# Optimization experiments

Hardware: AMD Instinct MI355X
Metric: run time of the kernel (lower is better)

Reference implementation:

```python
import jax, jax.numpy as jnp
import numpy as np

B, C, N = 4, 128, 25000
E = 200000            # edges per graph
H, DH = 4, 32         # heads, per-head dim
OUT = H * DH          # 128
ED = 32               # edge feature dim


def setup_inputs() -> dict:
    key = jax.random.key(0)
    ks = jax.random.split(key, 16)
    s = 0.05
    return {
        'x': jax.random.normal(ks[0], (B, C, N, 1), jnp.float32),
        'edge_index': jax.random.randint(ks[1], (B, 2, E), 0, B * N, jnp.int64),
        'edge_attr': jax.random.normal(ks[2], (B * E, ED), jnp.float32),
        'Wq': jax.random.normal(ks[3], (C, OUT), jnp.float32) * s,
        'bq': jnp.zeros((OUT,), jnp.float32),
        'Wk': jax.random.normal(ks[4], (C, OUT), jnp.float32) * s,
        'bk': jnp.zeros((OUT,), jnp.float32),
        'Wv': jax.random.normal(ks[5], (C, OUT), jnp.float32) * s,
        'bv': jnp.zeros((OUT,), jnp.float32),
        'We': jax.random.normal(ks[6], (ED, OUT), jnp.float32) * s,
        'Wskip': jax.random.normal(ks[7], (C, OUT), jnp.float32) * s,
        'bskip': jnp.zeros((OUT,), jnp.float32),
        'W1': jax.random.normal(ks[8], (OUT, 2 * OUT), jnp.float32) * s,
        'b1': jnp.zeros((2 * OUT,), jnp.float32),
        'W2': jax.random.normal(ks[9], (2 * OUT, OUT), jnp.float32) * s,
        'b2': jnp.zeros((OUT,), jnp.float32),
    }


def reference(x, edge_index, edge_attr, Wq, bq, Wk, bk, Wv, bv, We,
              Wskip, bskip, W1, b1, W2, b2):
    b, c, n, _ = x.shape
    nb = b * n
    # [B,C,N,1] -> [B*N, C]
    xf = x.squeeze(-1).transpose(0, 2, 1).reshape(nb, c)
    # [B,2,E] -> [2, B*E]
    ei = edge_index.transpose(1, 0, 2).reshape(2, -1)
    src, dst = ei[0], ei[1]

    q = (xf @ Wq + bq).reshape(nb, H, DH)
    k = (xf @ Wk + bk).reshape(nb, H, DH)
    v = (xf @ Wv + bv).reshape(nb, H, DH)
    e = (edge_attr @ We).reshape(-1, H, DH)  # [T,H,DH]

    qi = q[dst]            # gather target queries  [T,H,DH]
    kj = k[src] + e        # gather source keys + edge proj
    vj = v[src] + e

    scale = 1.0 / np.sqrt(DH).astype(np.float32)
    alpha = (qi * kj).sum(-1) * scale  # [T,H]

    # segment softmax over edges sharing a destination node
    amax = jax.ops.segment_max(alpha, dst, num_segments=nb)
    amax = jnp.where(jnp.isfinite(amax), amax, 0.0)
    ea = jnp.exp(alpha - amax[dst])
    denom = jax.ops.segment_sum(ea, dst, num_segments=nb)
    attn = ea / (denom[dst] + 1e-16)   # [T,H]

    agg = jax.ops.segment_sum(vj * attn[..., None], dst, num_segments=nb)
    out = agg.reshape(nb, OUT) + (xf @ Wskip + bskip)  # root skip

    # feed-forward + final activation
    h = jnp.maximum(out @ W1 + b1, 0.0) @ W2 + b2
    h = jnp.maximum(h, 0.0)

    # [B*N, OUT] -> [B, OUT, N, 1]
    return h.reshape(b, n, OUT).transpose(0, 2, 1)[..., None]
```

## Files before the change

### kernel.cpp

```cpp
#include <hip/hip_runtime.h>
#include <hip/hip_bf16.h>

#define NB      100000
#define NPB     25000
#define T_E     800000
#define EPG     200000
#define DMODEL  128
#define EDIM    32
#define FFD     256
#define SCAN_NBLK 98

typedef __attribute__((ext_vector_type(8))) short bf16x8;
typedef __attribute__((ext_vector_type(4))) float f32x4;
typedef __attribute__((ext_vector_type(2))) float f32x2;

__device__ inline unsigned short f2bf(float f) {
    unsigned u = __float_as_uint(f);
    unsigned r = u + 0x7fffu + ((u >> 16) & 1u);
    return (unsigned short)(r >> 16);
}
__device__ inline unsigned pack_bf16x2(float lo, float hi) {
    return (unsigned)f2bf(lo) | ((unsigned)f2bf(hi) << 16);
}
__device__ inline float bf_lo(unsigned p) { return __uint_as_float(p << 16); }
__device__ inline float bf_hi(unsigned p) { return __uint_as_float(p & 0xffff0000u); }

__global__ __launch_bounds__(256) void k_prep(
    const float* __restrict__ W1, const float* __restrict__ W2,
    const float* __restrict__ We,
    const float* __restrict__ Wq, const float* __restrict__ Wk,
    const float* __restrict__ Wv, const float* __restrict__ Wskip,
    uint4* __restrict__ w1f, uint4* __restrict__ w2f,
    uint4* __restrict__ wef, uint4* __restrict__ wpf)
{
    int t = blockIdx.x * 256 + threadIdx.x;
    int lane = t & 63;
    int frag = t >> 6;
    if (frag >= 264) return;
    int rl = lane & 15, g = lane >> 4;
    unsigned v[4];
    if (frag < 64) {
        int m1 = frag >> 2, ks = frag & 3;
        int col1 = m1 * 16 + rl;
        int k0 = ks * 32 + g * 8;
#pragma unroll
        for (int j2 = 0; j2 < 4; ++j2) {
            float f0 = W1[(k0 + 2 * j2) * FFD + col1];
            float f1 = W1[(k0 + 2 * j2 + 1) * FFD + col1];
            v[j2] = pack_bf16x2(f0, f1);
        }
        w1f[frag * 64 + lane] = make_uint4(v[0], v[1], v[2], v[3]);
    } else if (frag < 128) {
        int f2 = frag - 64;
        int m2 = f2 >> 3, ks = f2 & 7;
        int c2 = m2 * 16 + rl;
        int k0 = ks * 32 + g * 8;
#pragma unroll
        for (int j2 = 0; j2 < 4; ++j2) {
            float f0 = W2[(k0 + 2 * j2) * DMODEL + c2];
            float f1 = W2[(k0 + 2 * j2 + 1) * DMODEL + c2];
            v[j2] = pack_bf16x2(f0, f1);
        }
        w2f[f2 * 64 + lane] = make_uint4(v[0], v[1], v[2], v[3]);
    } else if (frag < 136) {
        int m = frag - 128;
        int ocol = m * 16 + rl;
        int k0 = g * 8;
#pragma unroll
        for (int j2 = 0; j2 < 4; ++j2) {
            float f0 = We[(k0 + 2 * j2) * DMODEL + ocol];
            float f1 = We[(k0 + 2 * j2 + 1) * DMODEL + ocol];
            v[j2] = pack_bf16x2(f0, f1);
        }
        wef[m * 64 + lane] = make_uint4(v[0], v[1], v[2], v[3]);
    } else {
        int fi = frag - 136;
        int m  = fi >> 5;
        int r  = fi & 31;
        int ct = r >> 2, ks = r & 3;
        const float* W = (m == 0) ? Wq : (m == 1) ? Wk : (m == 2) ? Wv : Wskip;
        int col = ct * 16 + rl;
        int k0  = ks * 32 + g * 8;
#pragma unroll
        for (int j2 = 0; j2 < 4; ++j2) {
            float f0 = W[(k0 + 2 * j2) * DMODEL + col];
            float f1 = W[(k0 + 2 * j2 + 1) * DMODEL + col];
            v[j2] = pack_bf16x2(f0, f1);
        }
        wpf[fi * 64 + lane] = make_uint4(v[0], v[1], v[2], v[3]);
    }
}

#define STG 16384

__global__ __launch_bounds__(256) void k_proj2(
    const float* __restrict__ x, const uint4* __restrict__ wpf,
    const float* __restrict__ bq, const float* __restrict__ bk,
    const float* __restrict__ bv, const float* __restrict__ bskip,
    unsigned short* __restrict__ qb16, unsigned short* __restrict__ kvb,
    unsigned short* __restrict__ skipb16)
{
    __shared__ __align__(16) char lds[32768];
    const int tid   = threadIdx.x;
    const int node0 = blockIdx.x * 64;

    {
        const int nl   = tid & 63;
        const int half = tid >> 6;
        const int node = node0 + nl;
        const bool valid = node < NB;
        int b  = node / NPB;
        int nn = node - b * NPB;
        const float* xbase = x + (size_t)b * DMODEL * NPB + nn;
#pragma unroll
        for (int o = 0; o < 4; ++o) {
            int c0 = (half * 4 + o) * 8;
            unsigned vals[4];
#pragma unroll
            for (int j2 = 0; j2 < 4; ++j2) {
                float f0 = valid ? xbase[(size_t)(c0 + 2 * j2) * NPB] : 0.f;
                float f1 = valid ? xbase[(size_t)(c0 + 2 * j2 + 1) * NPB] : 0.f;
                vals[j2] = pack_bf16x2(f0, f1);
            }
            int byte = nl * 256 + ((c0 * 2) ^ ((nl & 7) << 4));
            *(uint4*)(&lds[byte]) = make_uint4(vals[0], vals[1], vals[2], vals[3]);
        }
    }
    __syncthreads();

    const int w = tid >> 6, lane = tid & 63;
    const int rl = lane & 15, g = lane >> 4;

    for (int m = 0; m < 4; ++m) {
        const float* bi = (m == 0) ? bq : (m == 1) ? bk : (m == 2) ? bv : bskip;
#pragma unroll
        for (int ct2 = 0; ct2 < 2; ++ct2) {
            const int ct = w * 2 + ct2;
            bf16x8 A[4];
#pragma unroll
            for (int ks = 0; ks < 4; ++ks)
                A[ks] = *(const bf16x8*)&wpf[((m * 8 + ct) * 4 + ks) * 64 + lane];
            const int colb = ct * 16 + g * 4;
            const float bb0 = bi[colb], bb1 = bi[colb + 1],
                        bb2 = bi[colb + 2], bb3 = bi[colb + 3];
#pragma unroll
            for (int nt = 0; nt < 4; ++nt) {
                const int nl = nt * 16 + rl;
                f32x4 acc = {0.f, 0.f, 0.f, 0.f};
#pragma unroll
                for (int ks = 0; ks < 4; ++ks) {
                    bf16x8 B = *(const bf16x8*)(&lds[nl * 256 +
                                  ((ks * 64 + g * 16) ^ ((nl & 7) << 4))]);
                    acc = __builtin_amdgcn_mfma_f32_16x16x32_bf16(A[ks], B, acc, 0, 0, 0);
                }
                unsigned lo = pack_bf16x2(acc[0] + bb0, acc[1] + bb1);
                unsigned hi = pack_bf16x2(acc[2] + bb2, acc[3] + bb3);
                int byte = STG + nl * 256 + ((colb * 2) ^ ((nl & 7) << 4));
                *(uint2*)(&lds[byte]) = make_uint2(lo, hi);
            }
        }
        __syncthreads();
#pragma unroll
        for (int i = 0; i < 4; ++i) {
            int linear = i * 256 + tid;
            int row = linear >> 4;
            int c8  = (linear & 15) * 8;
            int node = node0 + row;
            if (node < NB) {
                uint4 vv = *(const uint4*)(&lds[STG + row * 256 +
                                ((c8 * 2) ^ ((row & 7) << 4))]);
                if (m == 0)      *(uint4*)&qb16[(size_t)node * DMODEL + c8] = vv;
                else if (m == 1) *(uint4*)&kvb[(size_t)node * 256 + c8] = vv;
                else if (m == 2) *(uint4*)&kvb[(size_t)node * 256 + 128 + c8] = vv;
                else             *(uint4*)&skipb16[(size_t)node * DMODEL + c8] = vv;
            }
        }
        __syncthreads();
    }
}

__global__ __launch_bounds__(256) void k_hist(
    const int* __restrict__ eidx, int* __restrict__ counts)
{
    int t = blockIdx.x * 256 + threadIdx.x;
    if (t < T_E) {
        int b = t / EPG, e = t - b * EPG;
        int dst = eidx[(size_t)(b * 2 + 1) * EPG + e];
        atomicAdd(&counts[dst], 1);
    }
}

__global__ __launch_bounds__(1024) void k_scan1(
    const int* __restrict__ counts, int* __restrict__ row_start,
    int* __restrict__ bsum)
{
    __shared__ int s[1024];
    const int tid = threadIdx.x;
    const int gid = blockIdx.x * 1024 + tid;
    int v = (gid < NB) ? counts[gid] : 0;
    s[tid] = v;
    __syncthreads();
#pragma unroll
    for (int off = 1; off < 1024; off <<= 1) {
        int tv = (tid >= off) ? s[tid - off] : 0;
        __syncthreads();
        s[tid] += tv;
        __syncthreads();
    }
    int incl = s[tid];
    if (gid < NB) row_start[gid] = incl - v;
    if (tid == 1023) bsum[blockIdx.x] = incl;
}

__global__ __launch_bounds__(128) void k_scan2(int* __restrict__ bsum)
{
    __shared__ int s[128];
    const int tid = threadIdx.x;
    int v = (tid < SCAN_NBLK) ? bsum[tid] : 0;
    s[tid] = v;
    __syncthreads();
#pragma unroll
    for (int off = 1; off < 128; off <<= 1) {
        int tv = (tid >= off) ? s[tid - off] : 0;
        __syncthreads();
        s[tid] += tv;
        __syncthreads();
    }
    if (tid < SCAN_NBLK) bsum[tid] = s[tid] - v;
}

__global__ __launch_bounds__(1024) void k_scan3(
    int* __restrict__ row_start, const int* __restrict__ bsum,
    int* __restrict__ cursor)
{
    const int gid = blockIdx.x * 1024 + threadIdx.x;
    if (gid < NB) {
        int v = row_start[gid] + bsum[blockIdx.x];
        row_start[gid] = v;
        cursor[gid] = v;
    }
}

__global__ __launch_bounds__(256) void k_escat(
    const float* __restrict__ eattr, const uint4* __restrict__ wef,
    const int* __restrict__ eidx, int* __restrict__ cursor,
    unsigned char* __restrict__ eb, int2* __restrict__ elist2)
{
    const int tid = threadIdx.x;
    const int w = tid >> 6, lane = tid & 63;
    const int rl = lane & 15, g = lane >> 4;

    bf16x8 a[8];
#pragma unroll
    for (int m = 0; m < 8; ++m) a[m] = *(const bf16x8*)&wef[m * 64 + lane];

    const int nwaves = gridDim.x * 4;
    for (int tile = blockIdx.x * 4 + w; tile < T_E / 16; tile += nwaves) {
        const float* ep = &eattr[((size_t)tile * 16 + rl) * EDIM + g * 8];
        float4 f0 = *(const float4*)ep;
        float4 f1 = *(const float4*)(ep + 4);
        uint4 bu = make_uint4(pack_bf16x2(f0.x, f0.y), pack_bf16x2(f0.z, f0.w),
                              pack_bf16x2(f1.x, f1.y), pack_bf16x2(f1.z, f1.w));
        bf16x8 b = *(bf16x8*)&bu;
        f32x4 z = {0.f, 0.f, 0.f, 0.f};
        f32x4 acc[8];
#pragma unroll
        for (int m = 0; m < 8; ++m)
            acc[m] = __builtin_amdgcn_mfma_f32_16x16x32_bf16(a[m], b, z, 0, 0, 0);
        unsigned char* out = &eb[((size_t)tile * 16 + rl) * DMODEL + g * 4];
#pragma unroll
        for (int m = 0; m < 8; ++m) {
            unsigned d = __builtin_amdgcn_cvt_pk_fp8_f32(acc[m][0], acc[m][1], 0, false);
            d = __builtin_amdgcn_cvt_pk_fp8_f32(acc[m][2], acc[m][3], d, true);
            *(unsigned*)(out + m * 16) = d;
        }
        if (g == 0) {
            int t = tile * 16 + rl;
            int bb = t / EPG, e = t - bb * EPG;
            int dst = eidx[(size_t)(bb * 2 + 1) * EPG + e];
            int src = eidx[(size_t)(bb * 2) * EPG + e];
            int pos = atomicAdd(&cursor[dst], 1);
            elist2[pos] = make_int2(src, t);
        }
    }
}

__global__ __launch_bounds__(256) void k_aggr3(
    unsigned short* qx,
    const unsigned short* __restrict__ kvb,
    const unsigned short* __restrict__ skipb16,
    const unsigned char* __restrict__ eb,
    const int2* __restrict__ elist2,
    const int* __restrict__ row_start, const int* __restrict__ row_end)
{
    const int tid = threadIdx.x;
    const int w = tid >> 6, l = tid & 63;
    const int q4 = l >> 4;
    const int li = l & 15;
    const int c0 = li * 8;

    const int nwaves = gridDim.x * 4;
    for (int node = blockIdx.x * 4 + w; node < NB; node += nwaves) {
        const int rs = row_start[node];
        const int re = row_end[node];
        uint4 qp = *(const uint4*)&qx[(size_t)node * DMODEL + c0];
        const float q0 = bf_lo(qp.x), q1 = bf_hi(qp.x);
        const float q2 = bf_lo(qp.y), q3 = bf_hi(qp.y);
        const float q4_ = bf_lo(qp.z), q5 = bf_hi(qp.z);
        const float q6 = bf_lo(qp.w), q7 = bf_hi(qp.w);
        float a0 = 0.f, a1 = 0.f, a2 = 0.f, a3 = 0.f;
        float a4 = 0.f, a5 = 0.f, a6 = 0.f, a7 = 0.f, den = 0.f;

        for (int j0 = rs; j0 < re; j0 += 8) {
            const int jcA = j0 + q4;
            const int jcB = j0 + 4 + q4;
            const bool actA = jcA < re;
            const bool actB = jcB < re;
            uint4 kpA = make_uint4(0,0,0,0), vpA = make_uint4(0,0,0,0);
            uint4 kpB = make_uint4(0,0,0,0), vpB = make_uint4(0,0,0,0);
            uint2 epA = make_uint2(0,0), epB = make_uint2(0,0);
            if (actA) {
                int2 se = elist2[jcA];
                kpA = *(const uint4*)&kvb[(size_t)se.x * 256 + c0];
                vpA = *(const uint4*)&kvb[(size_t)se.x * 256 + 128 + c0];
                epA = *(const uint2*)&eb[(size_t)se.y * DMODEL + c0];
            }
            if (actB) {
                int2 se = elist2[jcB];
                kpB = *(const uint4*)&kvb[(size_t)se.x * 256 + c0];
                vpB = *(const uint4*)&kvb[(size_t)se.x * 256 + 128 + c0];
                epB = *(const uint2*)&eb[(size_t)se.y * DMODEL + c0];
            }
            {
                f32x2 exl = __builtin_amdgcn_cvt_pk_f32_fp8(epA.x, false);
                f32x2 exh = __builtin_amdgcn_cvt_pk_f32_fp8(epA.x, true);
                f32x2 eyl = __builtin_amdgcn_cvt_pk_f32_fp8(epA.y, false);
                f32x2 eyh = __builtin_amdgcn_cvt_pk_f32_fp8(epA.y, true);
                const float e0 = exl[0], e1 = exl[1], e2 = exh[0], e3 = exh[1];
                const float e4 = eyl[0], e5 = eyl[1], e6 = eyh[0], e7 = eyh[1];
                float p = q0 * (bf_lo(kpA.x) + e0) + q1 * (bf_hi(kpA.x) + e1)
                        + q2 * (bf_lo(kpA.y) + e2) + q3 * (bf_hi(kpA.y) + e3)
                        + q4_ * (bf_lo(kpA.z) + e4) + q5 * (bf_hi(kpA.z) + e5)
                        + q6 * (bf_lo(kpA.w) + e6) + q7 * (bf_hi(kpA.w) + e7);
                p += __shfl_xor(p, 1, 64);
                p += __shfl_xor(p, 2, 64);
                float ea = actA ? __expf(p * 0.17677669529663689f) : 0.f;
                a0 += ea * (bf_lo(vpA.x) + e0);  a1 += ea * (bf_hi(vpA.x) + e1);
                a2 += ea * (bf_lo(vpA.y) + e2);  a3 += ea * (bf_hi(vpA.y) + e3);
                a4 += ea * (bf_lo(vpA.z) + e4);  a5 += ea * (bf_hi(vpA.z) + e5);
                a6 += ea * (bf_lo(vpA.w) + e6);  a7 += ea * (bf_hi(vpA.w) + e7);
                den += ea;
            }
            {
                f32x2 exl = __builtin_amdgcn_cvt_pk_f32_fp8(epB.x, false);
                f32x2 exh = __builtin_amdgcn_cvt_pk_f32_fp8(epB.x, true);
                f32x2 eyl = __builtin_amdgcn_cvt_pk_f32_fp8(epB.y, false);
                f32x2 eyh = __builtin_amdgcn_cvt_pk_f32_fp8(epB.y, true);
                const float e0 = exl[0], e1 = exl[1], e2 = exh[0], e3 = exh[1];
                const float e4 = eyl[0], e5 = eyl[1], e6 = eyh[0], e7 = eyh[1];
                float p = q0 * (bf_lo(kpB.x) + e0) + q1 * (bf_hi(kpB.x) + e1)
                        + q2 * (bf_lo(kpB.y) + e2) + q3 * (bf_hi(kpB.y) + e3)
                        + q4_ * (bf_lo(kpB.z) + e4) + q5 * (bf_hi(kpB.z) + e5)
                        + q6 * (bf_lo(kpB.w) + e6) + q7 * (bf_hi(kpB.w) + e7);
                p += __shfl_xor(p, 1, 64);
                p += __shfl_xor(p, 2, 64);
                float ea = actB ? __expf(p * 0.17677669529663689f) : 0.f;
                a0 += ea * (bf_lo(vpB.x) + e0);  a1 += ea * (bf_hi(vpB.x) + e1);
                a2 += ea * (bf_lo(vpB.y) + e2);  a3 += ea * (bf_hi(vpB.y) + e3);
                a4 += ea * (bf_lo(vpB.z) + e4);  a5 += ea * (bf_hi(vpB.z) + e5);
                a6 += ea * (bf_lo(vpB.w) + e6);  a7 += ea * (bf_hi(vpB.w) + e7);
                den += ea;
            }
        }
#pragma unroll
        for (int off = 16; off <= 32; off <<= 1) {
            a0 += __shfl_xor(a0, off, 64);  a1 += __shfl_xor(a1, off, 64);
            a2 += __shfl_xor(a2, off, 64);  a3 += __shfl_xor(a3, off, 64);
            a4 += __shfl_xor(a4, off, 64);  a5 += __shfl_xor(a5, off, 64);
            a6 += __shfl_xor(a6, off, 64);  a7 += __shfl_xor(a7, off, 64);
            den += __shfl_xor(den, off, 64);
        }
        float r = 1.0f / (den + 1e-16f);
        if (q4 == 0) {
            uint4 sp = *(const uint4*)&skipb16[(size_t)node * DMODEL + c0];
            uint4 o;
            o.x = pack_bf16x2(a0 * r + bf_lo(sp.x), a1 * r + bf_hi(sp.x));
            o.y = pack_bf16x2(a2 * r + bf_lo(sp.y), a3 * r + bf_hi(sp.y));
            o.z = pack_bf16x2(a4 * r + bf_lo(sp.z), a5 * r + bf_hi(sp.z));
            o.w = pack_bf16x2(a6 * r + bf_lo(sp.w), a7 * r + bf_hi(sp.w));
            *(uint4*)&qx[(size_t)node * DMODEL + c0] = o;
        }
    }
}

#define H1_OFF 16384

__global__ __launch_bounds__(256) void k_ffn_mfma(
    const unsigned short* __restrict__ xs16,
    const uint4* __restrict__ w1f, const float* __restrict__ b1,
    const uint4* __restrict__ w2f, const float* __restrict__ b2,
    float* __restrict__ out)
{
    __shared__ __align__(16) char lds[49152];
    const int tid   = threadIdx.x;
    const int node0 = blockIdx.x * 64;

#pragma unroll
    for (int i = 0; i < 4; ++i) {
        int linear = i * 256 + tid;
        int row = linear >> 4;
        int c8  = (linear & 15) * 8;
        int node = node0 + row;
        uint4 vv = (node < NB) ? *(const uint4*)&xs16[(size_t)node * DMODEL + c8]
                               : make_uint4(0, 0, 0, 0);
        int byte = row * 256 + ((c8 * 2) ^ ((row & 7) << 4));
        *(uint4*)(&lds[byte]) = vv;
    }
    __syncthreads();

    const int w = tid >> 6, lane = tid & 63;
    const int rl = lane & 15, g = lane >> 4;

    {
        f32x4 acc[4][4] = {};
#pragma unroll
        for (int ks = 0; ks < 4; ++ks) {
            bf16x8 a[4], b[4];
#pragma unroll
            for (int mt = 0; mt < 4; ++mt) {
                int m1 = w * 4 + mt;
                a[mt] = *(const bf16x8*)&w1f[(m1 * 4 + ks) * 64 + lane];
            }
#pragma unroll
            for (int nt = 0; nt < 4; ++nt) {
                int node = nt * 16 + rl;
                int byte = node * 256 + ((ks * 64 + g * 16) ^ ((node & 7) << 4));
                b[nt] = *(const bf16x8*)&lds[byte];
            }
#pragma unroll
            for (int mt = 0; mt < 4; ++mt)
#pragma unroll
                for (int nt = 0; nt < 4; ++nt)
                    acc[mt][nt] = __builtin_amdgcn_mfma_f32_16x16x32_bf16(
                        a[mt], b[nt], acc[mt][nt], 0, 0, 0);
        }
#pragma unroll
        for (int mt = 0; mt < 4; ++mt) {
            int col1_0 = w * 64 + mt * 16 + g * 4;
            float bb0 = b1[col1_0], bb1 = b1[col1_0 + 1],
                  bb2 = b1[col1_0 + 2], bb3 = b1[col1_0 + 3];
#pragma unroll
            for (int nt = 0; nt < 4; ++nt) {
                int node = nt * 16 + rl;
                float v0 = fmaxf(acc[mt][nt][0] + bb0, 0.f);
                float v1 = fmaxf(acc[mt][nt][1] + bb1, 0.f);
                float v2 = fmaxf(acc[mt][nt][2] + bb2, 0.f);
                float v3 = fmaxf(acc[mt][nt][3] + bb3, 0.f);
                unsigned lo = pack_bf16x2(v0, v1), hi = pack_bf16x2(v2, v3);
                int byte = H1_OFF + node * 512 + ((col1_0 * 2) ^ ((node & 7) << 4));
                *(uint2*)(&lds[byte]) = make_uint2(lo, hi);
            }
        }
    }
    __syncthreads();

    {
        f32x4 acc[2][4] = {};
#pragma unroll
        for (int ks = 0; ks < 8; ++ks) {
            bf16x8 a[2], b[4];
#pragma unroll
            for (int mt = 0; mt < 2; ++mt) {
                int m2 = w * 2 + mt;
                a[mt] = *(const bf16x8*)&w2f[(m2 * 8 + ks) * 64 + lane];
            }
#pragma unroll
            for (int nt = 0; nt < 4; ++nt) {
                int node = nt * 16 + rl;
                int byte = H1_OFF + node * 512 + ((ks * 64 + g * 16) ^ ((node & 7) << 4));
                b[nt] = *(const bf16x8*)&lds[byte];
            }
#pragma unroll
            for (int mt = 0; mt < 2; ++mt)
#pragma unroll
                for (int nt = 0; nt < 4; ++nt)
                    acc[mt][nt] = __builtin_amdgcn_mfma_f32_16x16x32_bf16(
                        a[mt], b[nt], acc[mt][nt], 0, 0, 0);
        }
#pragma unroll
        for (int mt = 0; mt < 2; ++mt) {
            int c2_0 = w * 32 + mt * 16 + g * 4;
#pragma unroll
            for (int nt = 0; nt < 4; ++nt) {
                int node = node0 + nt * 16 + rl;
                if (node < NB) {
                    int bb = node / NPB;
                    int nn = node - bb * NPB;
                    size_t base = (size_t)(bb * DMODEL) * NPB + nn;
#pragma unroll
                    for (int r = 0; r < 4; ++r) {
                        float v = fmaxf(acc[mt][nt][r] + b2[c2_0 + r], 0.f);
                        out[base + (size_t)(c2_0 + r) * NPB] = v;
                    }
                }
            }
        }
    }
}

extern "C" void kernel_launch(void* const* d_in, const int* in_sizes, int n_in,
                              void* d_out, int out_size, void* d_ws, size_t ws_size,
                              hipStream_t stream)
{
    const float* x     = (const float*)d_in[0];
    const int*   eidx  = (const int*)  d_in[1];
    const float* eattr = (const float*)d_in[2];
    const float* Wq    = (const float*)d_in[3];
    const float* bq    = (const float*)d_in[4];
    const float* Wk    = (const float*)d_in[5];
    const float* bk    = (const float*)d_in[6];
    const float* Wv    = (const float*)d_in[7];
    const float* bv    = (const float*)d_in[8];
    const float* We    = (const float*)d_in[9];
    const float* Wskip = (const float*)d_in[10];
    const float* bskip = (const float*)d_in[11];
    const float* W1    = (const float*)d_in[12];
    const float* b1    = (const float*)d_in[13];
    const float* W2    = (const float*)d_in[14];
    const float* b2    = (const float*)d_in[15];
    float* out = (float*)d_out;

    const size_t NBD = (size_t)NB * DMODEL;
    unsigned short* qb16    = (unsigned short*)d_ws;
    unsigned short* kvb     = qb16 + NBD;
    unsigned short* skipb16 = kvb + 2 * NBD;
    unsigned char*  eb      = (unsigned char*)(skipb16 + NBD);
    uint4* w1f = (uint4*)(eb + (size_t)T_E * DMODEL);
    uint4* w2f = w1f + 64 * 64;
    uint4* wef = w2f + 64 * 64;
    uint4* wpf = wef + 8 * 64;
    int* counts    = (int*)(wpf + 128 * 64);
    int* row_start = counts + NB;
    int* cursor    = row_start + NB;
    int2* elist2   = (int2*)(cursor + NB);
    int* bsum      = (int*)(elist2 + T_E);

    hipMemsetAsync(counts, 0, NB * sizeof(int), stream);
    k_prep<<<66, 256, 0, stream>>>(W1, W2, We, Wq, Wk, Wv, Wskip,
                                   w1f, w2f, wef, wpf);
    k_proj2<<<(NB + 63) / 64, 256, 0, stream>>>(x, wpf, bq, bk, bv, bskip,
                                                qb16, kvb, skipb16);
    k_hist<<<(T_E + 255) / 256, 256, 0, stream>>>(eidx, counts);
    k_scan1<<<SCAN_NBLK, 1024, 0, stream>>>(counts, row_start, bsum);
    k_scan2<<<1, 128, 0, stream>>>(bsum);
    k_scan3<<<SCAN_NBLK, 1024, 0, stream>>>(row_start, bsum, cursor);
    k_escat<<<2048, 256, 0, stream>>>(eattr, wef, eidx, cursor, eb, elist2);
    k_aggr3<<<2048, 256, 0, stream>>>(qb16, kvb, skipb16, eb, elist2,
                                      row_start, cursor);
    k_ffn_mfma<<<(NB + 63) / 64, 256, 0, stream>>>(qb16, w1f, b1, w2f, b2, out);
}
```

Measured before the change: 340.3 us.

## Split edge scatter from edge projection and stage FP8 output through swizzled LDS

Moves the atomic CSR scatter into its own fully parallel kernel with one thread per edge, instead of running it on only a quarter of the lanes inside the MFMA edge-projection loop. The edge projection now writes its FP8 results into an XOR-swizzled LDS tile and then stores them as coalesced 16-byte rows, replacing scattered 4-byte global stores. This adds one kernel launch and an LDS round trip per tile.

After: 303.0 us. 11.0% less time.

```diff
diff --git a/kernel.cpp b/kernel.cpp
--- a/kernel.cpp
+++ b/kernel.cpp
@@ -241,14 +241,29 @@
     }
 }
 
-__global__ __launch_bounds__(256) void k_escat(
+__global__ __launch_bounds__(256) void k_scatter(
+    const int* __restrict__ eidx, int* __restrict__ cursor,
+    int2* __restrict__ elist2)
+{
+    int t = blockIdx.x * 256 + threadIdx.x;
+    if (t < T_E) {
+        int b = t / EPG, e = t - b * EPG;
+        int dst = eidx[(size_t)(b * 2 + 1) * EPG + e];
+        int src = eidx[(size_t)(b * 2) * EPG + e];
+        int pos = atomicAdd(&cursor[dst], 1);
+        elist2[pos] = make_int2(src, t);
+    }
+}
+
+__global__ __launch_bounds__(256) void k_eproj(
     const float* __restrict__ eattr, const uint4* __restrict__ wef,
-    const int* __restrict__ eidx, int* __restrict__ cursor,
-    unsigned char* __restrict__ eb, int2* __restrict__ elist2)
-{
+    unsigned char* __restrict__ eb)
+{
+    __shared__ __align__(16) char elds[8192];
     const int tid = threadIdx.x;
     const int w = tid >> 6, lane = tid & 63;
     const int rl = lane & 15, g = lane >> 4;
+    char* myl = &elds[w * 2048];
 
     bf16x8 a[8];
 #pragma unroll
@@ -267,20 +282,18 @@
 #pragma unroll
         for (int m = 0; m < 8; ++m)
             acc[m] = __builtin_amdgcn_mfma_f32_16x16x32_bf16(a[m], b, z, 0, 0, 0);
-        unsigned char* out = &eb[((size_t)tile * 16 + rl) * DMODEL + g * 4];
 #pragma unroll
         for (int m = 0; m < 8; ++m) {
             unsigned d = __builtin_amdgcn_cvt_pk_fp8_f32(acc[m][0], acc[m][1], 0, false);
             d = __builtin_amdgcn_cvt_pk_fp8_f32(acc[m][2], acc[m][3], d, true);
-            *(unsigned*)(out + m * 16) = d;
-        }
-        if (g == 0) {
-            int t = tile * 16 + rl;
-            int bb = t / EPG, e = t - bb * EPG;
-            int dst = eidx[(size_t)(bb * 2 + 1) * EPG + e];
-            int src = eidx[(size_t)(bb * 2) * EPG + e];
-            int pos = atomicAdd(&cursor[dst], 1);
-            elist2[pos] = make_int2(src, t);
+            *(unsigned*)(myl + rl * 128 + ((m * 16) ^ ((rl & 7) << 4)) + g * 4) = d;
+        }
+#pragma unroll
+        for (int it = 0; it < 2; ++it) {
+            int lin = it * 64 + lane;
+            int row = lin >> 3, chunk = lin & 7;
+            uint4 vv = *(const uint4*)(myl + row * 128 + ((chunk ^ (row & 7)) << 4));
+            *(uint4*)&eb[(size_t)tile * 2048 + (size_t)lin * 16] = vv;
         }
     }
 }
@@ -554,7 +567,8 @@
     k_scan1<<<SCAN_NBLK, 1024, 0, stream>>>(counts, row_start, bsum);
     k_scan2<<<1, 128, 0, stream>>>(bsum);
     k_scan3<<<SCAN_NBLK, 1024, 0, stream>>>(row_start, bsum, cursor);
-    k_escat<<<2048, 256, 0, stream>>>(eattr, wef, eidx, cursor, eb, elist2);
+    k_scatter<<<(T_E + 255) / 256, 256, 0, stream>>>(eidx, cursor, elist2);
+    k_eproj<<<2048, 256, 0, stream>>>(eattr, wef, eb);
     k_aggr3<<<2048, 256, 0, stream>>>(qb16, kvb, skipb16, eb, elist2,
                                       row_start, cursor);
     k_ffn_mfma<<<(NB + 63) / 64, 256, 0, stream>>>(qb16, w1f, b1, w2f, b2, out);
```
